# Kernel optimization log

Hardware: AMD Instinct MI355X
Metric: run time of the kernel (lower is better)

The kernel has to match this reference:

```python
import jax, jax.numpy as jnp
import numpy as np

N = 100_000      # nodes
E = 1_600_000    # edges (avg degree 16)
IN, HID, H1, OUT = 128, 16, 8, 64


def setup_inputs() -> dict:
    key = jax.random.key(0)
    ks = jax.random.split(key, 11)
    s = 0.1
    return {
        "x":   jax.random.normal(ks[0], (N, IN), jnp.float32),
        "src": jax.random.randint(ks[1], (E,), 0, N),
        "dst": jax.random.randint(ks[2], (E,), 0, N),
        "W1":  jax.random.normal(ks[3], (IN, H1 * HID), jnp.float32) * s,
        "al1": jax.random.normal(ks[4], (H1, HID), jnp.float32) * s,
        "ar1": jax.random.normal(ks[5], (H1, HID), jnp.float32) * s,
        "b1":  jnp.zeros((H1 * HID,), jnp.float32),
        "W2":  jax.random.normal(ks[6], (H1 * HID, OUT), jnp.float32) * s,
        "al2": jax.random.normal(ks[7], (1, OUT), jnp.float32) * s,
        "ar2": jax.random.normal(ks[8], (1, OUT), jnp.float32) * s,
        "b2":  jnp.zeros((OUT,), jnp.float32),
    }


def gat_layer(h, W, al, ar, b, src, dst, heads, dim, act):
    # DGL GATConv (eval mode, no dropout, no residual)
    feat = (h @ W).reshape(-1, heads, dim)               # (N, H, D)
    el = jnp.einsum('nhd,hd->nh', feat, al)              # (N, H)
    er = jnp.einsum('nhd,hd->nh', feat, ar)              # (N, H)
    e = jax.nn.leaky_relu(el[src] + er[dst], 0.2)        # (E, H)
    # edge softmax over incoming edges of each dst node
    m = jax.ops.segment_max(e, dst, num_segments=N)      # (N, H)
    m = jnp.where(jnp.isfinite(m), m, 0.0)               # isolated nodes
    ex = jnp.exp(e - m[dst])                             # (E, H)
    denom = jax.ops.segment_sum(ex, dst, num_segments=N) # (N, H)
    alpha = ex / jnp.maximum(denom[dst], 1e-9)           # (E, H)
    msg = feat[src] * alpha[:, :, None]                  # (E, H, D) -- dominant traffic
    rst = jax.ops.segment_sum(msg, dst, num_segments=N)  # (N, H, D)
    rst = rst + b.reshape(1, heads, dim)
    return act(rst) if act is not None else rst


def reference(x, src, dst, W1, al1, ar1, b1, W2, al2, ar2, b2):
    h = gat_layer(x, W1, al1, ar1, b1, src, dst, H1, HID, jax.nn.elu)
    h = h.reshape(N, H1 * HID)                           # flatten heads
    out = gat_layer(h, W2, al2, ar2, b2, src, dst, 1, OUT, None)
    return out.mean(axis=1)                              # mean over heads -> (N, OUT)
```

## Files before the change

kernel.cpp:

```cpp
#include <hip/hip_runtime.h>
#include <hip/hip_bf16.h>


#define NN 100000
#define NE 1600000
#define NB 391
#define NBK 98

typedef unsigned short u16;
typedef unsigned int   u32;
typedef __attribute__((ext_vector_type(4))) float f32x4;
typedef __attribute__((ext_vector_type(8))) short short8;

__device__ __forceinline__ float bf2f(u16 u) { return __uint_as_float(((u32)u) << 16); }
__device__ __forceinline__ float bflo(u32 u) { return __uint_as_float(u << 16); }
__device__ __forceinline__ float bfhi(u32 u) { return __uint_as_float(u & 0xffff0000u); }
__device__ __forceinline__ u16 f2bf(float f) {
    u32 u = __float_as_uint(f);
    return (u16)((u + 0x7fffu + ((u >> 16) & 1u)) >> 16);
}
__device__ __forceinline__ float lrelu(float v) { return v > 0.f ? v : 0.2f * v; }
__device__ __forceinline__ float loadf(const void* p, size_t i, int isf32) {
    return isf32 ? ((const float*)p)[i] : bf2f(((const u16*)p)[i]);
}

__global__ void k_detect(const u16* __restrict__ x, int* __restrict__ flag)
{
    __shared__ float s[256];
    int t = threadIdx.x;
    float a = 0.f;
    for (int i = t; i < 1024; i += 256) a += fminf(fabsf(bf2f(x[i])), 1e6f);
    s[t] = a;
    __syncthreads();
    if (t == 0) {
        float tot = 0.f;
        for (int i = 0; i < 256; ++i) tot += s[i];
        *flag = (tot * (1.f / 1024.f) > 100.f) ? 1 : 0;
    }
}

__global__ void k_beacon(u16* __restrict__ out, int n, float code)
{
    int tid = blockIdx.x * 256 + threadIdx.x;
    if (tid < n) out[tid] = f2bf(code);
}

__global__ __launch_bounds__(256) void k_prep(
    const void* __restrict__ W1, const void* __restrict__ W2,
    const int* __restrict__ flag, u16* __restrict__ W1T, u16* __restrict__ W2T)
{
    int i = blockIdx.x * 256 + threadIdx.x;
    int isf32 = *flag;
    if (i < 16384) {
        int k = i >> 7, n = i & 127;
        W1T[n * 128 + k] = isf32 ? f2bf(((const float*)W1)[i]) : ((const u16*)W1)[i];
    } else if (i < 24576) {
        int j = i - 16384;
        int k = j >> 6, n = j & 63;
        W2T[n * 128 + k] = isf32 ? f2bf(((const float*)W2)[j]) : ((const u16*)W2)[j];
    }
}

__global__ __launch_bounds__(256) void k_gemm1m(
    const void* __restrict__ x, const u16* __restrict__ W1T,
    const void* __restrict__ al1, const void* __restrict__ ar1,
    const int* __restrict__ flag,
    u16* __restrict__ hC, float* __restrict__ el1, float* __restrict__ er1)
{
    __shared__ __align__(16) char smem[52224];
    __shared__ float alS[128], arS[128];
    u16* xT = (u16*)smem;
    u16* wT = (u16*)(smem + 17408);
    float* fB = (float*)smem;

    const int t  = threadIdx.x;
    const int r0 = blockIdx.x * 64;
    const int isf32 = *flag;

    if (t < 128) { alS[t] = loadf(al1, t, isf32); arS[t] = loadf(ar1, t, isf32); }

    {
        const uint4* wg = (const uint4*)W1T;
        #pragma unroll
        for (int it = 0; it < 8; ++it) {
            int idx = t + it * 256;
            int r = idx >> 4, k = (idx & 15) * 8;
            *(uint4*)&wT[r * 136 + k] = wg[idx];
        }
    }
    if (!isf32) {
        const u16* xg = (const u16*)x;
        #pragma unroll
        for (int it = 0; it < 4; ++it) {
            int idx = t + it * 256;
            int r = idx >> 4, k = (idx & 15) * 8;
            int rr = r0 + r; if (rr >= NN) rr = NN - 1;
            *(uint4*)&xT[r * 136 + k] = *(const uint4*)&xg[(size_t)rr * 128 + k];
        }
    } else {
        const float* xg = (const float*)x;
        #pragma unroll
        for (int it = 0; it < 8; ++it) {
            int idx = t + it * 256;
            int r = idx >> 5, k = (idx & 31) * 4;
            int rr = r0 + r; if (rr >= NN) rr = NN - 1;
            float4 v = *(const float4*)&xg[(size_t)rr * 128 + k];
            ushort4 o; o.x = f2bf(v.x); o.y = f2bf(v.y); o.z = f2bf(v.z); o.w = f2bf(v.w);
            *(ushort4*)&xT[r * 136 + k] = o;
        }
    }
    __syncthreads();

    const int w = t >> 6, lane = t & 63;
    const int lm = lane & 15, lk = (lane >> 4) * 8;
    const u16* aP = &xT[(w * 16 + lm) * 136 + lk];
    const u16* bP = &wT[lm * 136 + lk];

    f32x4 acc[8];
    #pragma unroll
    for (int i = 0; i < 8; ++i) acc[i] = (f32x4){0.f, 0.f, 0.f, 0.f};

    #pragma unroll
    for (int ks = 0; ks < 4; ++ks) {
        short8 a = *(const short8*)(aP + ks * 32);
        #pragma unroll
        for (int ct = 0; ct < 8; ++ct) {
            short8 b = *(const short8*)(bP + ct * 16 * 136 + ks * 32);
            acc[ct] = __builtin_amdgcn_mfma_f32_16x16x32_bf16(a, b, acc[ct], 0, 0, 0);
        }
    }
    __syncthreads();

    {
        int rbase = w * 16 + (lane >> 4) * 4;
        #pragma unroll
        for (int ct = 0; ct < 8; ++ct) {
            #pragma unroll
            for (int r = 0; r < 4; ++r)
                fB[(rbase + r) * 132 + ct * 16 + lm] = acc[ct][r];
        }
    }
    __syncthreads();

    #pragma unroll
    for (int it = 0; it < 16; ++it) {
        int idx = t + it * 256;
        int r = idx >> 6, c2 = (idx & 63) * 2;
        int rr = r0 + r;
        if (rr < NN) {
            u32 pk = (u32)f2bf(fB[r * 132 + c2]) | ((u32)f2bf(fB[r * 132 + c2 + 1]) << 16);
            *(u32*)&hC[(size_t)rr * 128 + c2] = pk;
        }
    }
    #pragma unroll
    for (int p = 0; p < 2; ++p) {
        int task = t + p * 256;
        int r = task >> 3, hh = task & 7;
        float el = 0.f, er = 0.f;
        #pragma unroll
        for (int dd = 0; dd < 16; ++dd) {
            float f = fB[r * 132 + hh * 16 + dd];
            el += f * alS[hh * 16 + dd];
            er += f * arS[hh * 16 + dd];
        }
        int rr = r0 + r;
        if (rr < NN) { el1[rr * 8 + hh] = el; er1[rr * 8 + hh] = er; }
    }
}

__global__ __launch_bounds__(256) void k_gemm2m(
    const u16* __restrict__ hT, const u16* __restrict__ hHi,
    const u16* __restrict__ W2T,
    const void* __restrict__ al2, const void* __restrict__ ar2,
    const int* __restrict__ flag,
    u16* __restrict__ feat2, float* __restrict__ el2, float* __restrict__ er2)
{
    __shared__ __align__(16) char smem[34816];
    __shared__ float alS[64], arS[64];
    u16* xT = (u16*)smem;
    u16* wT = (u16*)(smem + 17408);
    float* fB = (float*)smem;

    const int t  = threadIdx.x;
    const int r0 = blockIdx.x * 64;
    const int isf32 = *flag;

    if (t < 64) { alS[t] = loadf(al2, t, isf32); arS[t] = loadf(ar2, t, isf32); }

    {
        const uint4* wg = (const uint4*)W2T;
        #pragma unroll
        for (int it = 0; it < 4; ++it) {
            int idx = t + it * 256;
            int r = idx >> 4, k = (idx & 15) * 8;
            *(uint4*)&wT[r * 136 + k] = wg[idx];
        }
    }
    #pragma unroll
    for (int it = 0; it < 4; ++it) {
        int idx = t + it * 256;
        int r = idx >> 4, j = idx & 15;
        int rr = r0 + r; if (rr >= NN) rr = NN - 1;
        const u16* sp = (j < 8) ? &hT[(size_t)rr * 64 + j * 8]
                                : &hHi[(size_t)rr * 128 + (j - 8) * 8];
        *(uint4*)&xT[r * 136 + j * 8] = *(const uint4*)sp;
    }
    __syncthreads();

    const int w = t >> 6, lane = t & 63;
    const int lm = lane & 15, lk = (lane >> 4) * 8;
    const u16* aP = &xT[(w * 16 + lm) * 136 + lk];
    const u16* bP = &wT[lm * 136 + lk];

    f32x4 acc[4];
    #pragma unroll
    for (int i = 0; i < 4; ++i) acc[i] = (f32x4){0.f, 0.f, 0.f, 0.f};

    #pragma unroll
    for (int ks = 0; ks < 4; ++ks) {
        short8 a = *(const short8*)(aP + ks * 32);
        #pragma unroll
        for (int ct = 0; ct < 4; ++ct) {
            short8 b = *(const short8*)(bP + ct * 16 * 136 + ks * 32);
            acc[ct] = __builtin_amdgcn_mfma_f32_16x16x32_bf16(a, b, acc[ct], 0, 0, 0);
        }
    }
    __syncthreads();

    {
        int rbase = w * 16 + (lane >> 4) * 4;
        #pragma unroll
        for (int ct = 0; ct < 4; ++ct) {
            #pragma unroll
            for (int r = 0; r < 4; ++r)
                fB[(rbase + r) * 68 + ct * 16 + lm] = acc[ct][r];
        }
    }
    __syncthreads();

    #pragma unroll
    for (int it = 0; it < 8; ++it) {
        int idx = t + it * 256;
        int r = idx >> 5, c2 = (idx & 31) * 2;
        int rr = r0 + r;
        if (rr < NN) {
            u32 pk = (u32)f2bf(fB[r * 68 + c2]) | ((u32)f2bf(fB[r * 68 + c2 + 1]) << 16);
            *(u32*)&feat2[(size_t)rr * 128 + c2] = pk;
        }
    }
    {
        int r = t >> 2, q = t & 3;
        float el = 0.f, er = 0.f;
        #pragma unroll
        for (int dd = 0; dd < 16; ++dd) {
            float f = fB[r * 68 + q * 16 + dd];
            el += f * alS[q * 16 + dd];
            er += f * arS[q * 16 + dd];
        }
        el += __shfl_xor(el, 1); el += __shfl_xor(el, 2);
        er += __shfl_xor(er, 1); er += __shfl_xor(er, 2);
        int rr = r0 + r;
        if (q == 0 && rr < NN) { el2[rr] = el; er2[rr] = er; }
    }
}


__global__ __launch_bounds__(256) void k_cnt(
    const int* __restrict__ dst, int* __restrict__ gcnt)
{
    __shared__ int cnt[NBK];
    const int t = threadIdx.x;
    if (t < NBK) cnt[t] = 0;
    __syncthreads();
    const int e0 = blockIdx.x * 4096 + t;
    #pragma unroll
    for (int i = 0; i < 16; ++i) {
        int e = e0 + i * 256;
        if (e < NE) atomicAdd(&cnt[dst[e] >> 10], 1);
    }
    __syncthreads();
    if (t < NBK) gcnt[blockIdx.x * NBK + t] = cnt[t];
}

__global__ __launch_bounds__(512) void k_scan1(
    int* __restrict__ gcnt, int* __restrict__ total)
{
    __shared__ int s[512];
    const int t = threadIdx.x, k = blockIdx.x;
    int c = (t < NB) ? gcnt[t * NBK + k] : 0;
    s[t] = c; __syncthreads();
    for (int off = 1; off < 512; off <<= 1) {
        int v = (t >= off) ? s[t - off] : 0;
        __syncthreads();
        s[t] += v;
        __syncthreads();
    }
    if (t < NB) gcnt[t * NBK + k] = s[t] - c;
    if (t == NB - 1) total[k] = s[t];
}

__global__ __launch_bounds__(128) void k_scan2(
    const int* __restrict__ total, int* __restrict__ bstart)
{
    __shared__ int s[128];
    const int t = threadIdx.x;
    int c = (t < NBK) ? total[t] : 0;
    s[t] = c; __syncthreads();
    for (int off = 1; off < 128; off <<= 1) {
        int v = (t >= off) ? s[t - off] : 0;
        __syncthreads();
        s[t] += v;
        __syncthreads();
    }
    if (t < NBK) bstart[t] = s[t] - c;
    if (t == NBK - 1) bstart[NBK] = s[t];
}

__global__ __launch_bounds__(256) void k_part(
    const int* __restrict__ src, const int* __restrict__ dst,
    const int* __restrict__ gcnt, const int* __restrict__ bstart,
    u32* __restrict__ pair)
{
    __shared__ int cnt[NBK];
    __shared__ int gb[NBK];
    const int t = threadIdx.x;
    const int e0 = blockIdx.x * 4096 + t;

    if (t < NBK) cnt[t] = 0;
    __syncthreads();

    int sv[16], dv[16], rk[16];
    #pragma unroll
    for (int i = 0; i < 16; ++i) {
        int e = e0 + i * 256;
        if (e < NE) {
            sv[i] = src[e];
            dv[i] = dst[e];
            rk[i] = atomicAdd(&cnt[dv[i] >> 10], 1);
        }
    }
    __syncthreads();
    if (t < NBK) gb[t] = bstart[t] + gcnt[blockIdx.x * NBK + t];
    __syncthreads();

    #pragma unroll
    for (int i = 0; i < 16; ++i) {
        int e = e0 + i * 256;
        if (e < NE) {
            u32 p = ((u32)(dv[i] & 1023) << 17) | (u32)sv[i];
            pair[gb[dv[i] >> 10] + rk[i]] = p;
        }
    }
}

__global__ __launch_bounds__(256) void k_build(
    const u32* __restrict__ pair, const int* __restrict__ bstart,
    int* __restrict__ ptr, int* __restrict__ csr_src)
{
    __shared__ int cur[1024];
    __shared__ int part[256];
    const int t = threadIdx.x;
    const int b = blockIdx.x;
    const int r0 = b << 10;
    const int nloc = min(1024, NN - r0);
    const int bs = bstart[b], be = bstart[b + 1];

    for (int i = t; i < 1024; i += 256) cur[i] = 0;
    __syncthreads();

    for (int e = bs + t; e < be; e += 256)
        atomicAdd(&cur[pair[e] >> 17], 1);
    __syncthreads();

    int t4 = t * 4;
    int c0 = cur[t4], c1 = cur[t4 + 1], c2 = cur[t4 + 2], c3 = cur[t4 + 3];
    int sum = c0 + c1 + c2 + c3;
    part[t] = sum; __syncthreads();
    for (int off = 1; off < 256; off <<= 1) {
        int v = (t >= off) ? part[t - off] : 0;
        __syncthreads();
        part[t] += v;
        __syncthreads();
    }
    int basep = bs + part[t] - sum;
    cur[t4]     = basep;
    cur[t4 + 1] = basep + c0;
    cur[t4 + 2] = basep + c0 + c1;
    cur[t4 + 3] = basep + c0 + c1 + c2;
    __syncthreads();

    for (int e = bs + t; e < be; e += 256) {
        u32 p = pair[e];
        int pos = atomicAdd(&cur[p >> 17], 1);
        csr_src[pos] = (int)(p & 0x1FFFFu);
    }
    __syncthreads();

    for (int i = t; i < nloc; i += 256) ptr[r0 + i] = cur[i];
}

__global__ __launch_bounds__(256) void k_agg1c(
    const int* __restrict__ ptr, const int* __restrict__ csr_src,
    const float* __restrict__ el1, const float* __restrict__ er1,
    const u16* __restrict__ feat1,
    const void* __restrict__ b1, const int* __restrict__ flag,
    u16* __restrict__ outp, int ostride, int cb)
{
    const int wv = threadIdx.x >> 6, lane = threadIdx.x & 63;
    const int g = lane >> 3, ql = lane & 7;
    const int d = blockIdx.x * 32 + wv * 8 + g;
    const int c0 = cb + ql * 8;
    const int hh = c0 >> 4;

    float er_d = er1[d * 8 + hh];
    int start = d ? ptr[d - 1] : 0;
    int end   = ptr[d];

    float a0 = 0.f, a1 = 0.f, a2 = 0.f, a3 = 0.f;
    float a4 = 0.f, a5 = 0.f, a6 = 0.f, a7 = 0.f, wsum = 0.f;
    int i = start;
    while (i + 4 <= end) {
        int s0 = csr_src[i], s1 = csr_src[i + 1];
        int s2 = csr_src[i + 2], s3 = csr_src[i + 3];
        float e0 = el1[s0 * 8 + hh], e1 = el1[s1 * 8 + hh];
        float e2 = el1[s2 * 8 + hh], e3 = el1[s3 * 8 + hh];
        uint4 f0 = *(const uint4*)&feat1[(size_t)s0 * 128 + c0];
        uint4 f1 = *(const uint4*)&feat1[(size_t)s1 * 128 + c0];
        uint4 f2 = *(const uint4*)&feat1[(size_t)s2 * 128 + c0];
        uint4 f3 = *(const uint4*)&feat1[(size_t)s3 * 128 + c0];
        float w0 = __expf(lrelu(e0 + er_d));
        float w1 = __expf(lrelu(e1 + er_d));
        float w2 = __expf(lrelu(e2 + er_d));
        float w3 = __expf(lrelu(e3 + er_d));
        a0 += w0 * bflo(f0.x); a1 += w0 * bfhi(f0.x);
        a2 += w0 * bflo(f0.y); a3 += w0 * bfhi(f0.y);
        a4 += w0 * bflo(f0.z); a5 += w0 * bfhi(f0.z);
        a6 += w0 * bflo(f0.w); a7 += w0 * bfhi(f0.w);
        wsum += w0;
        a0 += w1 * bflo(f1.x); a1 += w1 * bfhi(f1.x);
        a2 += w1 * bflo(f1.y); a3 += w1 * bfhi(f1.y);
        a4 += w1 * bflo(f1.z); a5 += w1 * bfhi(f1.z);
        a6 += w1 * bflo(f1.w); a7 += w1 * bfhi(f1.w);
        wsum += w1;
        a0 += w2 * bflo(f2.x); a1 += w2 * bfhi(f2.x);
        a2 += w2 * bflo(f2.y); a3 += w2 * bfhi(f2.y);
        a4 += w2 * bflo(f2.z); a5 += w2 * bfhi(f2.z);
        a6 += w2 * bflo(f2.w); a7 += w2 * bfhi(f2.w);
        wsum += w2;
        a0 += w3 * bflo(f3.x); a1 += w3 * bfhi(f3.x);
        a2 += w3 * bflo(f3.y); a3 += w3 * bfhi(f3.y);
        a4 += w3 * bflo(f3.z); a5 += w3 * bfhi(f3.z);
        a6 += w3 * bflo(f3.w); a7 += w3 * bfhi(f3.w);
        wsum += w3;
        i += 4;
    }
    while (i < end) {
        int s0 = csr_src[i];
        float w0 = __expf(lrelu(el1[s0 * 8 + hh] + er_d));
        uint4 f0 = *(const uint4*)&feat1[(size_t)s0 * 128 + c0];
        a0 += w0 * bflo(f0.x); a1 += w0 * bfhi(f0.x);
        a2 += w0 * bflo(f0.y); a3 += w0 * bfhi(f0.y);
        a4 += w0 * bflo(f0.z); a5 += w0 * bfhi(f0.z);
        a6 += w0 * bflo(f0.w); a7 += w0 * bfhi(f0.w);
        wsum += w0;
        ++i;
    }
    float inv = 1.f / fmaxf(wsum, 1e-9f);
    int isf32 = *flag;
    float v0 = a0 * inv + loadf(b1, c0 + 0, isf32);
    float v1 = a1 * inv + loadf(b1, c0 + 1, isf32);
    float v2 = a2 * inv + loadf(b1, c0 + 2, isf32);
    float v3 = a3 * inv + loadf(b1, c0 + 3, isf32);
    float v4 = a4 * inv + loadf(b1, c0 + 4, isf32);
    float v5 = a5 * inv + loadf(b1, c0 + 5, isf32);
    float v6 = a6 * inv + loadf(b1, c0 + 6, isf32);
    float v7 = a7 * inv + loadf(b1, c0 + 7, isf32);
    v0 = v0 > 0.f ? v0 : expm1f(v0);
    v1 = v1 > 0.f ? v1 : expm1f(v1);
    v2 = v2 > 0.f ? v2 : expm1f(v2);
    v3 = v3 > 0.f ? v3 : expm1f(v3);
    v4 = v4 > 0.f ? v4 : expm1f(v4);
    v5 = v5 > 0.f ? v5 : expm1f(v5);
    v6 = v6 > 0.f ? v6 : expm1f(v6);
    v7 = v7 > 0.f ? v7 : expm1f(v7);
    uint4 o;
    o.x = (u32)f2bf(v0) | ((u32)f2bf(v1) << 16);
    o.y = (u32)f2bf(v2) | ((u32)f2bf(v3) << 16);
    o.z = (u32)f2bf(v4) | ((u32)f2bf(v5) << 16);
    o.w = (u32)f2bf(v6) | ((u32)f2bf(v7) << 16);
    *(uint4*)&outp[(size_t)d * ostride + ql * 8] = o;
}

__global__ __launch_bounds__(256) void k_agg2c(
    const int* __restrict__ ptr, const int* __restrict__ csr_src,
    const float* __restrict__ el2, const float* __restrict__ er2,
    const u16* __restrict__ feat2,
    const void* __restrict__ b2, const int* __restrict__ flag,
    void* __restrict__ out)
{
    const int wv = threadIdx.x >> 6, lane = threadIdx.x & 63;
    const int g = lane >> 3, ql = lane & 7;
    const int d = blockIdx.x * 32 + wv * 8 + g;
    const int c0 = ql * 8;

    float er_d = er2[d];
    int start = d ? ptr[d - 1] : 0;
    int end   = ptr[d];

    float a0 = 0.f, a1 = 0.f, a2 = 0.f, a3 = 0.f;
    float a4 = 0.f, a5 = 0.f, a6 = 0.f, a7 = 0.f, wsum = 0.f;
    int i = start;
    while (i + 4 <= end) {
        int s0 = csr_src[i], s1 = csr_src[i + 1];
        int s2 = csr_src[i + 2], s3 = csr_src[i + 3];
        float e0 = el2[s0], e1 = el2[s1], e2 = el2[s2], e3 = el2[s3];
        uint4 f0 = *(const uint4*)&feat2[(size_t)s0 * 128 + c0];
        uint4 f1 = *(const uint4*)&feat2[(size_t)s1 * 128 + c0];
        uint4 f2 = *(const uint4*)&feat2[(size_t)s2 * 128 + c0];
        uint4 f3 = *(const uint4*)&feat2[(size_t)s3 * 128 + c0];
        float w0 = __expf(lrelu(e0 + er_d));
        float w1 = __expf(lrelu(e1 + er_d));
        float w2 = __expf(lrelu(e2 + er_d));
        float w3 = __expf(lrelu(e3 + er_d));
        a0 += w0 * bflo(f0.x); a1 += w0 * bfhi(f0.x);
        a2 += w0 * bflo(f0.y); a3 += w0 * bfhi(f0.y);
        a4 += w0 * bflo(f0.z); a5 += w0 * bfhi(f0.z);
        a6 += w0 * bflo(f0.w); a7 += w0 * bfhi(f0.w);
        wsum += w0;
        a0 += w1 * bflo(f1.x); a1 += w1 * bfhi(f1.x);
        a2 += w1 * bflo(f1.y); a3 += w1 * bfhi(f1.y);
        a4 += w1 * bflo(f1.z); a5 += w1 * bfhi(f1.z);
        a6 += w1 * bflo(f1.w); a7 += w1 * bfhi(f1.w);
        wsum += w1;
        a0 += w2 * bflo(f2.x); a1 += w2 * bfhi(f2.x);
        a2 += w2 * bflo(f2.y); a3 += w2 * bfhi(f2.y);
        a4 += w2 * bflo(f2.z); a5 += w2 * bfhi(f2.z);
        a6 += w2 * bflo(f2.w); a7 += w2 * bfhi(f2.w);
        wsum += w2;
        a0 += w3 * bflo(f3.x); a1 += w3 * bfhi(f3.x);
        a2 += w3 * bflo(f3.y); a3 += w3 * bfhi(f3.y);
        a4 += w3 * bflo(f3.z); a5 += w3 * bfhi(f3.z);
        a6 += w3 * bflo(f3.w); a7 += w3 * bfhi(f3.w);
        wsum += w3;
        i += 4;
    }
    while (i < end) {
        int s0 = csr_src[i];
        float w0 = __expf(lrelu(el2[s0] + er_d));
        uint4 f0 = *(const uint4*)&feat2[(size_t)s0 * 128 + c0];
        a0 += w0 * bflo(f0.x); a1 += w0 * bfhi(f0.x);
        a2 += w0 * bflo(f0.y); a3 += w0 * bfhi(f0.y);
        a4 += w0 * bflo(f0.z); a5 += w0 * bfhi(f0.z);
        a6 += w0 * bflo(f0.w); a7 += w0 * bfhi(f0.w);
        wsum += w0;
        ++i;
    }
    float inv = 1.f / fmaxf(wsum, 1e-9f);
    int isf32 = *flag;
    float v0 = a0 * inv + loadf(b2, c0 + 0, isf32);
    float v1 = a1 * inv + loadf(b2, c0 + 1, isf32);
    float v2 = a2 * inv + loadf(b2, c0 + 2, isf32);
    float v3 = a3 * inv + loadf(b2, c0 + 3, isf32);
    float v4 = a4 * inv + loadf(b2, c0 + 4, isf32);
    float v5 = a5 * inv + loadf(b2, c0 + 5, isf32);
    float v6 = a6 * inv + loadf(b2, c0 + 6, isf32);
    float v7 = a7 * inv + loadf(b2, c0 + 7, isf32);
    size_t idx = (size_t)d * 64 + c0;
    if (isf32) {
        float4 oa; oa.x = v0; oa.y = v1; oa.z = v2; oa.w = v3;
        float4 ob; ob.x = v4; ob.y = v5; ob.z = v6; ob.w = v7;
        *(float4*)&((float*)out)[idx]     = oa;
        *(float4*)&((float*)out)[idx + 4] = ob;
    } else {
        uint4 o;
        o.x = (u32)f2bf(v0) | ((u32)f2bf(v1) << 16);
        o.y = (u32)f2bf(v2) | ((u32)f2bf(v3) << 16);
        o.z = (u32)f2bf(v4) | ((u32)f2bf(v5) << 16);
        o.w = (u32)f2bf(v6) | ((u32)f2bf(v7) << 16);
        *(uint4*)&((u16*)out)[idx] = o;
    }
}

extern "C" void kernel_launch(void* const* d_in, const int* in_sizes, int n_in,
                              void* d_out, int out_size, void* d_ws, size_t ws_size,
                              hipStream_t stream)
{
    static const int exp_sizes[11] = {12800000, 1600000, 1600000, 16384, 128, 128, 128, 8192, 64, 64, 64};
    float code = 0.f;
    if (n_in != 11) code = 9000.f;
    else {
        for (int i = 0; i < 11; ++i)
            if (in_sizes[i] != exp_sizes[i]) { code = 3000.f + 100.f * i; break; }
    }
    if (code == 0.f && out_size != 6400000) code = 7777.f;
    if (code == 0.f && ws_size < 46100000)  code = (float)(ws_size >> 20);
    if (code != 0.f) {
        k_beacon<<<(out_size + 255) / 256, 256, 0, stream>>>((u16*)d_out, out_size, code);
        return;
    }

    const void* x   = d_in[0];
    const int* src  = (const int*)d_in[1];
    const int* dst  = (const int*)d_in[2];
    const void* W1  = d_in[3];
    const void* al1 = d_in[4];
    const void* ar1 = d_in[5];
    const void* b1  = d_in[6];
    const void* W2  = d_in[7];
    const void* al2 = d_in[8];
    const void* ar2 = d_in[9];
    const void* b2  = d_in[10];

    char* base = (char*)d_ws;
    int*   flag  = (int*)   base;
    u16*   hC    = (u16*)  (base + 256);
    u16*   T     = (u16*)  (base + 25600256);
    u32*   pair  = (u32*)  (base + 25600256);
    int*   csr   = (int*)  (base + 38400256);
    int*   ptr   = (int*)  (base + 44800256);
    int*   gcnt  = (int*)  (base + 44800256);
    float* el2   = (float*)(base + 45200256);
    float* er2   = (float*)(base + 45600256);
    int*   total = (int*)  (base + 46000256);
    int*   bstart= (int*)  (base + 46002304);
    u16*   W1T   = (u16*)  (base + 46004352);
    u16*   W2T   = (u16*)  (base + 46037120);

    float* el1 = (float*)d_out;
    float* er1 = el1 + 800000;

    u16* hLo   = T;
    u16* hHi   = hC;
    u16* feat2 = hC + 64;

    k_detect<<<1, 256, 0, stream>>>((const u16*)x, flag);
    k_prep  <<<96, 256, 0, stream>>>(W1, W2, flag, W1T, W2T);

    k_gemm1m<<<1563, 256, 0, stream>>>(x, W1T, al1, ar1, flag, hC, el1, er1);

    k_cnt  <<<NB,  256, 0, stream>>>(dst, gcnt);
    k_scan1<<<NBK, 512, 0, stream>>>(gcnt, total);
    k_scan2<<<1,   128, 0, stream>>>(total, bstart);
    k_part <<<NB,  256, 0, stream>>>(src, dst, gcnt, bstart, pair);
    k_build<<<NBK, 256, 0, stream>>>(pair, bstart, ptr, csr);

    k_agg1c<<<3125, 256, 0, stream>>>(ptr, csr, el1, er1, hC, b1, flag, hLo, 64, 0);
    k_agg1c<<<3125, 256, 0, stream>>>(ptr, csr, el1, er1, hC, b1, flag, hHi, 128, 64);

    k_gemm2m<<<1563, 256, 0, stream>>>(hLo, hHi, W2T, al2, ar2, flag, feat2, el2, er2);

    k_agg2c<<<3125, 256, 0, stream>>>(ptr, csr, el2, er2, feat2, b2, flag, d_out);
}
```

Baseline: 339.8 us.

## Fuse destination-count pass into GEMM1 launch and use nontemporal CSR accesses

```diff
diff --git a/kernel.cpp b/kernel.cpp
--- a/kernel.cpp
+++ b/kernel.cpp
@@ -6,6 +6,7 @@
 #define NE 1600000
 #define NB 391
 #define NBK 98
+#define GEMM1_NB 1563
 
 typedef unsigned short u16;
 typedef unsigned int   u32;
@@ -65,15 +66,34 @@
     const void* __restrict__ x, const u16* __restrict__ W1T,
     const void* __restrict__ al1, const void* __restrict__ ar1,
     const int* __restrict__ flag,
-    u16* __restrict__ hC, float* __restrict__ el1, float* __restrict__ er1)
+    u16* __restrict__ hC, float* __restrict__ el1, float* __restrict__ er1,
+    const int* __restrict__ dst, int* __restrict__ gcnt)
 {
     __shared__ __align__(16) char smem[52224];
     __shared__ float alS[128], arS[128];
+
+    const int t = threadIdx.x;
+
+    if (blockIdx.x >= GEMM1_NB) {
+        int* cnt = (int*)smem;
+        const int b = blockIdx.x - GEMM1_NB;
+        if (t < NBK) cnt[t] = 0;
+        __syncthreads();
+        const int e0 = b * 4096 + t;
+        #pragma unroll
+        for (int ii = 0; ii < 16; ++ii) {
+            int e = e0 + ii * 256;
+            if (e < NE) atomicAdd(&cnt[dst[e] >> 10], 1);
+        }
+        __syncthreads();
+        if (t < NBK) gcnt[b * NBK + t] = cnt[t];
+        return;
+    }
+
     u16* xT = (u16*)smem;
     u16* wT = (u16*)(smem + 17408);
     float* fB = (float*)smem;
 
-    const int t  = threadIdx.x;
     const int r0 = blockIdx.x * 64;
     const int isf32 = *flag;
 
@@ -265,23 +285,6 @@
 }
 
 
-__global__ __launch_bounds__(256) void k_cnt(
-    const int* __restrict__ dst, int* __restrict__ gcnt)
-{
-    __shared__ int cnt[NBK];
-    const int t = threadIdx.x;
-    if (t < NBK) cnt[t] = 0;
-    __syncthreads();
-    const int e0 = blockIdx.x * 4096 + t;
-    #pragma unroll
-    for (int i = 0; i < 16; ++i) {
-        int e = e0 + i * 256;
-        if (e < NE) atomicAdd(&cnt[dst[e] >> 10], 1);
-    }
-    __syncthreads();
-    if (t < NBK) gcnt[blockIdx.x * NBK + t] = cnt[t];
-}
-
 __global__ __launch_bounds__(512) void k_scan1(
     int* __restrict__ gcnt, int* __restrict__ total)
 {
@@ -348,7 +351,7 @@
         int e = e0 + i * 256;
         if (e < NE) {
             u32 p = ((u32)(dv[i] & 1023) << 17) | (u32)sv[i];
-            pair[gb[dv[i] >> 10] + rk[i]] = p;
+            __builtin_nontemporal_store(p, &pair[gb[dv[i] >> 10] + rk[i]]);
         }
     }
 }
@@ -420,8 +423,10 @@
     float a4 = 0.f, a5 = 0.f, a6 = 0.f, a7 = 0.f, wsum = 0.f;
     int i = start;
     while (i + 4 <= end) {
-        int s0 = csr_src[i], s1 = csr_src[i + 1];
-        int s2 = csr_src[i + 2], s3 = csr_src[i + 3];
+        int s0 = __builtin_nontemporal_load(csr_src + i);
+        int s1 = __builtin_nontemporal_load(csr_src + i + 1);
+        int s2 = __builtin_nontemporal_load(csr_src + i + 2);
+        int s3 = __builtin_nontemporal_load(csr_src + i + 3);
         float e0 = el1[s0 * 8 + hh], e1 = el1[s1 * 8 + hh];
         float e2 = el1[s2 * 8 + hh], e3 = el1[s3 * 8 + hh];
         uint4 f0 = *(const uint4*)&feat1[(size_t)s0 * 128 + c0];
@@ -455,7 +460,7 @@
         i += 4;
     }
     while (i < end) {
-        int s0 = csr_src[i];
+        int s0 = __builtin_nontemporal_load(csr_src + i);
         float w0 = __expf(lrelu(el1[s0 * 8 + hh] + er_d));
         uint4 f0 = *(const uint4*)&feat1[(size_t)s0 * 128 + c0];
         a0 += w0 * bflo(f0.x); a1 += w0 * bfhi(f0.x);
@@ -511,8 +516,10 @@
     float a4 = 0.f, a5 = 0.f, a6 = 0.f, a7 = 0.f, wsum = 0.f;
     int i = start;
     while (i + 4 <= end) {
-        int s0 = csr_src[i], s1 = csr_src[i + 1];
-        int s2 = csr_src[i + 2], s3 = csr_src[i + 3];
+        int s0 = __builtin_nontemporal_load(csr_src + i);
+        int s1 = __builtin_nontemporal_load(csr_src + i + 1);
+        int s2 = __builtin_nontemporal_load(csr_src + i + 2);
+        int s3 = __builtin_nontemporal_load(csr_src + i + 3);
         float e0 = el2[s0], e1 = el2[s1], e2 = el2[s2], e3 = el2[s3];
         uint4 f0 = *(const uint4*)&feat2[(size_t)s0 * 128 + c0];
         uint4 f1 = *(const uint4*)&feat2[(size_t)s1 * 128 + c0];
@@ -545,7 +552,7 @@
         i += 4;
     }
     while (i < end) {
-        int s0 = csr_src[i];
+        int s0 = __builtin_nontemporal_load(csr_src + i);
         float w0 = __expf(lrelu(el2[s0] + er_d));
         uint4 f0 = *(const uint4*)&feat2[(size_t)s0 * 128 + c0];
         a0 += w0 * bflo(f0.x); a1 += w0 * bfhi(f0.x);
@@ -636,9 +643,9 @@
     k_detect<<<1, 256, 0, stream>>>((const u16*)x, flag);
     k_prep  <<<96, 256, 0, stream>>>(W1, W2, flag, W1T, W2T);
 
-    k_gemm1m<<<1563, 256, 0, stream>>>(x, W1T, al1, ar1, flag, hC, el1, er1);
-
-    k_cnt  <<<NB,  256, 0, stream>>>(dst, gcnt);
+    k_gemm1m<<<GEMM1_NB + NB, 256, 0, stream>>>(x, W1T, al1, ar1, flag, hC, el1, er1,
+                                                dst, gcnt);
+
     k_scan1<<<NBK, 512, 0, stream>>>(gcnt, total);
     k_scan2<<<1,   128, 0, stream>>>(total, bstart);
     k_part <<<NB,  256, 0, stream>>>(src, dst, gcnt, bstart, pair);
```

After: 382.6 us. 12.6% more time.
